# Kernel optimization log

Hardware: AMD Instinct MI355X
Metric: run time of the kernel (lower is better)

## Reference

```python
import jax, jax.numpy as jnp
import numpy as np

NUM_NODES = 50000
NUM_EDGES = 600000
NUM_FEAT = 128
HIDDEN = 512
N_OUT = 128
K = 3
N_GRAPHS = 128


def setup_inputs() -> dict:
    key = jax.random.key(0)
    ks = jax.random.split(key, 12)
    feature = jax.random.normal(ks[0], (NUM_NODES, NUM_FEAT), dtype=jnp.float32)
    edge_index = jax.random.randint(ks[1], (2, NUM_EDGES), 0, NUM_NODES, dtype=jnp.int64)
    protein_batch = jnp.sort(jax.random.randint(ks[2], (NUM_NODES,), 0, N_GRAPHS, dtype=jnp.int64))
    s = 0.05
    # ChebConv weights stored [K, in, out] (x @ W), single shared bias per conv
    W1 = jax.random.normal(ks[3], (K, NUM_FEAT, NUM_FEAT), dtype=jnp.float32) * s
    b1 = jax.random.normal(ks[4], (NUM_FEAT,), dtype=jnp.float32) * s
    W2 = jax.random.normal(ks[5], (K, NUM_FEAT, 2 * NUM_FEAT), dtype=jnp.float32) * s
    b2 = jax.random.normal(ks[6], (2 * NUM_FEAT,), dtype=jnp.float32) * s
    fc1_w = jax.random.normal(ks[7], (3 * NUM_FEAT, HIDDEN), dtype=jnp.float32) * s
    fc1_b = jax.random.normal(ks[8], (HIDDEN,), dtype=jnp.float32) * s
    fc2_w = jax.random.normal(ks[9], (HIDDEN, N_OUT), dtype=jnp.float32) * s
    fc2_b = jax.random.normal(ks[10], (N_OUT,), dtype=jnp.float32) * s
    return {"feature": feature, "edge_index": edge_index, "protein_batch": protein_batch,
            "W1": W1, "b1": b1, "W2": W2, "b2": b2,
            "fc1_w": fc1_w, "fc1_b": fc1_b, "fc2_w": fc2_w, "fc2_b": fc2_b}


def _cheb_conv(x, src, dst, edge_w, W, b):
    # PyG ChebConv with sym normalization, lambda_max=2 => scaled Laplacian
    # L_hat has zero diagonal and off-diag weights -1/sqrt(d_i d_j) (edge_w).
    def prop(h):
        return jax.ops.segment_sum(edge_w[:, None] * h[src], dst, num_segments=NUM_NODES)

    Tx0 = x
    out = Tx0 @ W[0]
    Tx1 = prop(x)
    out = out + Tx1 @ W[1]
    for k in range(2, W.shape[0]):
        Tx2 = 2.0 * prop(Tx1) - Tx0
        out = out + Tx2 @ W[k]
        Tx0, Tx1 = Tx1, Tx2
    return out + b


def reference(feature, edge_index, protein_batch, W1, b1, W2, b2, fc1_w, fc1_b, fc2_w, fc2_b):
    src, dst = edge_index[0], edge_index[1]
    deg = jax.ops.segment_sum(jnp.ones_like(src, dtype=feature.dtype), src, num_segments=NUM_NODES)
    dinv = jnp.where(deg > 0, jax.lax.rsqrt(jnp.maximum(deg, 1.0)), 0.0)
    edge_w = -dinv[src] * dinv[dst]  # (2/lambda_max)*L_sym off-diagonal; diag cancels to 0

    gx = jax.nn.relu(_cheb_conv(feature, src, dst, edge_w, W1, b1))
    gx = jax.nn.relu(_cheb_conv(gx, src, dst, edge_w, W2, b2))
    gx = jnp.concatenate([gx, feature], axis=1)  # [N, 3*F]

    # global_mean_pool
    sums = jax.ops.segment_sum(gx, protein_batch, num_segments=N_GRAPHS)
    cnts = jax.ops.segment_sum(jnp.ones((gx.shape[0],), gx.dtype), protein_batch, num_segments=N_GRAPHS)
    pooled = sums / jnp.maximum(cnts, 1.0)[:, None]

    h = jax.nn.relu(pooled @ fc1_w + fc1_b)  # dropout is identity in eval
    return h @ fc2_w + fc2_b
```

## Files before the change

kernel.cpp:

```cpp
#include <hip/hip_runtime.h>
#include <hip/hip_bf16.h>

#define NNODES 50000
#define NEDGES 600000
#define NB 196
#define NBKT 196
#define SB 192
#define SCH (NEDGES / SB)

typedef short vs8 __attribute__((ext_vector_type(8)));
typedef float floatx4 __attribute__((ext_vector_type(4)));

__device__ __forceinline__ float us2f(unsigned short u) {
    unsigned int x = ((unsigned int)u) << 16;
    float f;
    __builtin_memcpy(&f, &x, 4);
    return f;
}
__device__ __forceinline__ unsigned short f2us(float f) {
    unsigned int x;
    __builtin_memcpy(&x, &f, 4);
    unsigned int r = x + 0x7fffu + ((x >> 16) & 1u);
    return (unsigned short)(r >> 16);
}
__device__ __forceinline__ float ldf(const void* p, int i, int ff) {
    if (ff) return us2f(((const unsigned short*)p)[i]);
    return ((const float*)p)[i];
}
__device__ __forceinline__ int2 ldnt_sw(const int2* p) {
    unsigned long long v =
        __builtin_nontemporal_load(reinterpret_cast<const unsigned long long*>(p));
    int2 r;
    r.x = (int)(unsigned int)(v & 0xffffffffULL);
    r.y = (int)(unsigned int)(v >> 32);
    return r;
}
__device__ __forceinline__ void accum8(float w, uint4 u, float& a0, float& a1,
                                       float& a2, float& a3, float& a4, float& a5,
                                       float& a6, float& a7) {
    a0 += w * us2f((unsigned short)(u.x & 0xffffu));
    a1 += w * us2f((unsigned short)(u.x >> 16));
    a2 += w * us2f((unsigned short)(u.y & 0xffffu));
    a3 += w * us2f((unsigned short)(u.y >> 16));
    a4 += w * us2f((unsigned short)(u.z & 0xffffu));
    a5 += w * us2f((unsigned short)(u.z >> 16));
    a6 += w * us2f((unsigned short)(u.w & 0xffffu));
    a7 += w * us2f((unsigned short)(u.w >> 16));
}

__global__ void k_detect(const int* ei, const unsigned int* fw, int* iflag, int* fflag) {
    int lane = threadIdx.x;
    int odd1 = ei[2 * lane + 1];
    int odd2 = ei[128 + 2 * lane + 1];
    unsigned long long nz = __ballot(odd1 != 0 || odd2 != 0);
    unsigned int e = (fw[lane] >> 7) & 0xffu;
    unsigned long long h = __ballot(e > 100u && e < 160u);
    if (lane == 0) {
        *iflag = (nz == 0ULL) ? 1 : 0;
        *fflag = (__popcll(h) > 40) ? 1 : 0;
    }
}

__global__ void k_init(const int* pb, const int* iflag, int* b32, float* psum) {
    int i = blockIdx.x * 256 + threadIdx.x;
    if (i < NNODES) {
        int f = *iflag;
        b32[i] = pb[((size_t)i) << f];
    }
    if (i < 128 * 384) psum[i] = 0.f;
}

__global__ __launch_bounds__(256) void k_deghist(const int* ei, const int* iflag,
                                                 unsigned int* degpart, int* cntpart) {
    __shared__ unsigned int h[25000];
    __shared__ int c[NBKT];
    int t = threadIdx.x, blk = blockIdx.x;
    for (int i = t; i < 25000; i += 256) h[i] = 0u;
    if (t < NBKT) c[t] = 0;
    __syncthreads();
    int f = *iflag;
    int e0 = blk * SCH;
    for (int j = t; j < SCH; j += 256) {
        int e = e0 + j;
        int s = ei[((size_t)e) << f];
        int d = ei[((size_t)(NEDGES + e)) << f];
        atomicAdd(&h[s >> 1], (s & 1) ? 65536u : 1u);
        atomicAdd(&c[d >> 8], 1);
    }
    __syncthreads();
    unsigned int* dp = degpart + (size_t)blk * 25000;
    for (int i = t; i < 25000; i += 256) dp[i] = h[i];
    if (t < NBKT) cntpart[blk * NBKT + t] = c[t];
}

__global__ void k_dred(const unsigned int* degpart, float* dinv) {
    int i = blockIdx.x * 256 + threadIdx.x;
    if (i >= 25000) return;
    unsigned int lo = 0, hi = 0;
    for (int b = 0; b < SB; ++b) {
        unsigned int p = degpart[(size_t)b * 25000 + i];
        lo += p & 0xffffu;
        hi += p >> 16;
    }
    dinv[2 * i] = lo ? rsqrtf((float)lo) : 0.f;
    dinv[2 * i + 1] = hi ? rsqrtf((float)hi) : 0.f;
}

__global__ void k_bscan(const int* cntpart, int* bbase, int* gbase,
                        const int* batch32, int* pcnt, int* rowptr) {
    __shared__ int tot[256];
    int t = threadIdx.x;
    int sum = 0;
    if (t < NBKT) {
        for (int b = 0; b < SB; ++b) sum += cntpart[b * NBKT + t];
    }
    tot[t] = sum;
    __syncthreads();
    for (int off = 1; off < 256; off <<= 1) {
        int x = (t >= off) ? tot[t - off] : 0;
        __syncthreads();
        tot[t] += x;
        __syncthreads();
    }
    int excl = tot[t] - sum;
    if (t < NBKT) {
        gbase[t] = excl;
        int run = excl;
        for (int b = 0; b < SB; ++b) {
            bbase[b * NBKT + t] = run;
            run += cntpart[b * NBKT + t];
        }
    }
    if (t == 0) {
        gbase[NBKT] = NEDGES;
        rowptr[NNODES] = NEDGES;
    }
    if (t < 128) {
        int g = t;
        int lo = 0, hi = NNODES;
        while (lo < hi) { int mid = (lo + hi) >> 1; if (batch32[mid] < g) lo = mid + 1; else hi = mid; }
        int start = lo;
        hi = NNODES;
        while (lo < hi) { int mid = (lo + hi) >> 1; if (batch32[mid] <= g) lo = mid + 1; else hi = mid; }
        pcnt[g] = lo - start;
    }
}

__global__ void k_scat(const int* ei, const int* iflag, const float* dinv,
                       const int* bbase, int2* bkt) {
    __shared__ int cur[NBKT];
    int t = threadIdx.x, blk = blockIdx.x;
    if (t < NBKT) cur[t] = bbase[blk * NBKT + t];
    __syncthreads();
    int f = *iflag;
    int e0 = blk * SCH;
    for (int j = t; j < SCH; j += 256) {
        int e = e0 + j;
        int s = ei[((size_t)e) << f];
        int d = ei[((size_t)(NEDGES + e)) << f];
        float w = -dinv[s] * dinv[d];
        int slot = atomicAdd(&cur[d >> 8], 1);
        int wb;
        __builtin_memcpy(&wb, &w, 4);
        int2 v;
        v.x = s | ((d & 255) << 16);
        v.y = wb;
        bkt[slot] = v;
    }
}

__global__ void k_csr(const int2* bkt, const int* gbase, int* rowptr, int2* csr_sw) {
    __shared__ int hist[256], scan[256], cur[256];
    int t = threadIdx.x, b = blockIdx.x;
    int beg = gbase[b], end = gbase[b + 1];
    int n = end - beg;
    hist[t] = 0;
    __syncthreads();
    for (int i = t; i < n; i += 256) {
        int bin = (bkt[beg + i].x >> 16) & 255;
        atomicAdd(&hist[bin], 1);
    }
    __syncthreads();
    int h = hist[t];
    scan[t] = h;
    __syncthreads();
    for (int off = 1; off < 256; off <<= 1) {
        int x = (t >= off) ? scan[t - off] : 0;
        __syncthreads();
        scan[t] += x;
        __syncthreads();
    }
    int excl = scan[t] - h;
    int node = b * 256 + t;
    if (node < NNODES) rowptr[node] = beg + excl;
    cur[t] = excl;
    __syncthreads();
    for (int i = t; i < n; i += 256) {
        int2 p = bkt[beg + i];
        int bin = (p.x >> 16) & 255;
        int slot = atomicAdd(&cur[bin], 1);
        int2 v;
        v.x = p.x & 0xffff;
        v.y = p.y;
        csr_sw[beg + slot] = v;
    }
}

__global__ void k_featb(const void* src, const int* fflag, unsigned short* dst) {
    int i = blockIdx.x * 256 + threadIdx.x;
    if (i >= NNODES * 128 / 8) return;
    if (*fflag) {
        reinterpret_cast<uint4*>(dst)[i] = reinterpret_cast<const uint4*>(src)[i];
    } else {
        const float4* fs = reinterpret_cast<const float4*>(src);
        float4 a = fs[2 * i], b = fs[2 * i + 1];
        uint4 o;
        o.x = (unsigned int)f2us(a.x) | ((unsigned int)f2us(a.y) << 16);
        o.y = (unsigned int)f2us(a.z) | ((unsigned int)f2us(a.w) << 16);
        o.z = (unsigned int)f2us(b.x) | ((unsigned int)f2us(b.y) << 16);
        o.w = (unsigned int)f2us(b.z) | ((unsigned int)f2us(b.w) << 16);
        reinterpret_cast<uint4*>(dst)[i] = o;
    }
}

__global__ void k_trans2(const void* W1, const void* W2, const int* fflag,
                         unsigned short* W1t, unsigned short* W2t) {
    int idx = blockIdx.x * 256 + threadIdx.x;
    int ff = *fflag;
    if (idx < 49152) {
        int n = idx / 384, k = idx - n * 384;
        float v;
        if (k < 128) v = ldf(W1, k * 128 + n, ff) - ldf(W1, (256 + k) * 128 + n, ff);
        else if (k < 256) v = ldf(W1, k * 128 + n, ff);
        else v = 2.f * ldf(W1, k * 128 + n, ff);
        W1t[idx] = f2us(v);
    } else if (idx < 49152 + 98304) {
        int j = idx - 49152;
        int n = j / 384, k = j - n * 384;
        float v;
        if (k < 128) v = ldf(W2, k * 256 + n, ff) - ldf(W2, (256 + k) * 256 + n, ff);
        else if (k < 256) v = ldf(W2, k * 256 + n, ff);
        else v = 2.f * ldf(W2, k * 256 + n, ff);
        W2t[j] = f2us(v);
    }
}

__global__ void k_prepw(const void* b1, const void* b2, const void* f1w, const void* f1b,
                        const void* f2w, const void* f2b, const int* fflag,
                        float* b1f, float* b2f, float* f1wf, float* f1bf,
                        float* f2wf, float* f2bf) {
    int i = blockIdx.x * 256 + threadIdx.x;
    int ff = *fflag;
    if (i < 196608) { f1wf[i] = ldf(f1w, i, ff); return; }
    i -= 196608;
    if (i < 65536) { f2wf[i] = ldf(f2w, i, ff); return; }
    i -= 65536;
    if (i < 512) { f1bf[i] = ldf(f1b, i, ff); return; }
    i -= 512;
    if (i < 256) { b2f[i] = ldf(b2, i, ff); return; }
    i -= 256;
    if (i < 128) { b1f[i] = ldf(b1, i, ff); return; }
    i -= 128;
    if (i < 128) f2bf[i] = ldf(f2b, i, ff);
}

__global__ __launch_bounds__(256, 8) void k_prop(const unsigned short* X,
                                                 const int* rowptr, const int2* csr_sw,
                                                 unsigned short* out) {
    int wvid = (blockIdx.x * blockDim.x + threadIdx.x) >> 6;
    int lane = threadIdx.x & 63;
    int q = lane >> 4;
    int ln = lane & 15;
    int node = wvid * 4 + q;
    if (node >= NNODES) return;
    int fo = ln * 8;
    int beg = rowptr[node], end = rowptr[node + 1];
    float a0 = 0.f, a1 = 0.f, a2 = 0.f, a3 = 0.f;
    float a4 = 0.f, a5 = 0.f, a6 = 0.f, a7 = 0.f;
    int j = beg;
    for (; j + 4 <= end; j += 4) {
        int2 e0 = ldnt_sw(csr_sw + j);
        int2 e1 = ldnt_sw(csr_sw + j + 1);
        int2 e2 = ldnt_sw(csr_sw + j + 2);
        int2 e3 = ldnt_sw(csr_sw + j + 3);
        uint4 u0 = *reinterpret_cast<const uint4*>(X + (size_t)e0.x * 128 + fo);
        uint4 u1 = *reinterpret_cast<const uint4*>(X + (size_t)e1.x * 128 + fo);
        uint4 u2 = *reinterpret_cast<const uint4*>(X + (size_t)e2.x * 128 + fo);
        uint4 u3 = *reinterpret_cast<const uint4*>(X + (size_t)e3.x * 128 + fo);
        float w0, w1, w2, w3;
        __builtin_memcpy(&w0, &e0.y, 4);
        __builtin_memcpy(&w1, &e1.y, 4);
        __builtin_memcpy(&w2, &e2.y, 4);
        __builtin_memcpy(&w3, &e3.y, 4);
        accum8(w0, u0, a0, a1, a2, a3, a4, a5, a6, a7);
        accum8(w1, u1, a0, a1, a2, a3, a4, a5, a6, a7);
        accum8(w2, u2, a0, a1, a2, a3, a4, a5, a6, a7);
        accum8(w3, u3, a0, a1, a2, a3, a4, a5, a6, a7);
    }
    for (; j < end; ++j) {
        int2 e = ldnt_sw(csr_sw + j);
        float w;
        __builtin_memcpy(&w, &e.y, 4);
        uint4 u = *reinterpret_cast<const uint4*>(X + (size_t)e.x * 128 + fo);
        accum8(w, u, a0, a1, a2, a3, a4, a5, a6, a7);
    }
    uint4 ov;
    ov.x = (unsigned int)f2us(a0) | ((unsigned int)f2us(a1) << 16);
    ov.y = (unsigned int)f2us(a2) | ((unsigned int)f2us(a3) << 16);
    ov.z = (unsigned int)f2us(a4) | ((unsigned int)f2us(a5) << 16);
    ov.w = (unsigned int)f2us(a6) | ((unsigned int)f2us(a7) << 16);
    *reinterpret_cast<uint4*>(out + (size_t)node * 128 + fo) = ov;
}

template <int POOL, int NOUT>
__global__ __launch_bounds__(256, 6) void k_convg(
    const unsigned short* seg0, const unsigned short* seg1, const unsigned short* seg2,
    const unsigned short* Wt, const float* bias, unsigned short* out,
    const int* batch32, float* psum) {
    constexpr int SLABS = NOUT / 32;
    __shared__ unsigned short shb[12288];
    __shared__ float sh_ps[POOL ? 256 : 1];
    int tid = threadIdx.x;
    int bid = blockIdx.x;
    int grp = 8 * SLABS;
    int main_blocks = 24 * grp;
    int r, slab;
    if (bid < main_blocks) {
        int g = bid / grp;
        int rem = bid - g * grp;
        slab = rem >> 3;
        r = g * 8 + (rem & 7);
    } else {
        int t = bid - main_blocks;
        r = 192 + (t & 3);
        slab = t >> 2;
    }
    int col0 = slab * 32;
    if (POOL) sh_ps[tid] = 0.f;
#pragma unroll
    for (int it = 0; it < 6; ++it) {
        int idx = tid + it * 256;
        int kkt = idx >> 6, ln = idx & 63;
        int kk = kkt >> 1, t = kkt & 1;
        int col = col0 + t * 16 + (ln & 15);
        int ko = kk * 32 + (ln >> 4) * 8;
        uint4 v = *reinterpret_cast<const uint4*>(Wt + (size_t)col * 384 + ko);
        *reinterpret_cast<uint4*>(shb + idx * 8) = v;
    }
    __syncthreads();
    int wv = tid >> 6, lane = tid & 63;
    int m = lane & 15, kq = lane >> 4;
    int row0 = r * 256 + wv * 64;
    int rr[4];
#pragma unroll
    for (int mt = 0; mt < 4; ++mt) {
        int rw = row0 + mt * 16 + m;
        rr[mt] = rw < NNODES ? rw : NNODES - 1;
    }
    floatx4 acc[4][2];
#pragma unroll
    for (int mt = 0; mt < 4; ++mt)
#pragma unroll
        for (int t = 0; t < 2; ++t) {
            acc[mt][t][0] = 0.f; acc[mt][t][1] = 0.f;
            acc[mt][t][2] = 0.f; acc[mt][t][3] = 0.f;
        }
    const unsigned short* segs[3];
    segs[0] = seg0; segs[1] = seg1; segs[2] = seg2;
#pragma unroll
    for (int kk = 0; kk < 12; ++kk) {
        const unsigned short* S = segs[kk >> 2];
        int ko = (kk & 3) * 32 + kq * 8;
        vs8 a[4];
#pragma unroll
        for (int mt = 0; mt < 4; ++mt)
            a[mt] = *reinterpret_cast<const vs8*>(S + (size_t)rr[mt] * 128 + ko);
#pragma unroll
        for (int t = 0; t < 2; ++t) {
            vs8 b = *reinterpret_cast<const vs8*>(shb + ((kk * 2 + t) * 64 + lane) * 8);
#pragma unroll
            for (int mt = 0; mt < 4; ++mt)
                acc[mt][t] = __builtin_amdgcn_mfma_f32_16x16x32_bf16(a[mt], b, acc[mt][t], 0, 0, 0);
        }
    }
    if (POOL == 0) {
#pragma unroll
        for (int mt = 0; mt < 4; ++mt) {
            int rbase = row0 + mt * 16 + kq * 4;
#pragma unroll
            for (int t = 0; t < 2; ++t) {
                int col = col0 + t * 16 + m;
                float bv = bias[col];
#pragma unroll
                for (int i = 0; i < 4; ++i) {
                    int rw = rbase + i;
                    if (rw < NNODES) {
                        float v = acc[mt][t][i] + bv;
                        v = v > 0.f ? v : 0.f;
                        out[(size_t)rw * NOUT + col] = f2us(v);
                    }
                }
            }
        }
    } else {
        int g0 = batch32[r * 256];
#pragma unroll
        for (int mt = 0; mt < 4; ++mt) {
            int rbase = row0 + mt * 16 + kq * 4;
            int gid[4];
#pragma unroll
            for (int i = 0; i < 4; ++i) {
                int rw = rbase + i;
                gid[i] = rw < NNODES ? batch32[rw] : -1;
            }
#pragma unroll
            for (int t = 0; t < 2; ++t) {
                int col = col0 + t * 16 + m;
                float bv = bias[col];
                float run = 0.f;
                int curg = -1;
#pragma unroll
                for (int i = 0; i < 4; ++i) {
                    int g = gid[i];
                    if (g < 0) break;
                    float v = acc[mt][t][i] + bv;
                    v = v > 0.f ? v : 0.f;
                    if (g != curg) {
                        if (curg >= 0) {
                            int gl = curg - g0;
                            if (gl >= 0 && gl < 8) atomicAdd(&sh_ps[gl * 32 + t * 16 + m], run);
                            else atomicAdd(&psum[curg * 384 + col], run);
                        }
                        curg = g;
                        run = 0.f;
                    }
                    run += v;
                }
                if (curg >= 0) {
                    int gl = curg - g0;
                    if (gl >= 0 && gl < 8) atomicAdd(&sh_ps[gl * 32 + t * 16 + m], run);
                    else atomicAdd(&psum[curg * 384 + col], run);
                }
            }
        }
        __syncthreads();
        int gl = tid >> 5, c = tid & 31;
        float v = sh_ps[tid];
        int gg = g0 + gl;
        if (v != 0.f && gg < 128) atomicAdd(&psum[(size_t)gg * 384 + col0 + c], v);
    }
}

__global__ void k_poolnodes(const unsigned short* featb, const int* batch32, float* psum) {
    int col = threadIdx.x & 127;
    int half = threadIdx.x >> 7;
    int nbeg = blockIdx.x * 128 + half * 64;
    if (nbeg >= NNODES) return;
    int nend = nbeg + 64;
    if (nend > NNODES) nend = NNODES;
    float run = 0.f;
    int curg = batch32[nbeg];
    for (int n = nbeg; n < nend; ++n) {
        int g = batch32[n];
        if (g != curg) {
            atomicAdd(&psum[curg * 384 + 256 + col], run);
            run = 0.f;
            curg = g;
        }
        run += us2f(featb[(size_t)n * 128 + col]);
    }
    atomicAdd(&psum[curg * 384 + 256 + col], run);
}

__global__ void k_fc1(const float* psum, const int* pcnt, const float* w,
                      const float* b, float* h) {
    int g = blockIdx.x, j = threadIdx.x * 2;
    int c = pcnt[g];
    float inv = 1.f / (float)(c > 0 ? c : 1);
    float a0 = 0.f, a1 = 0.f;
    for (int k = 0; k < 384; ++k) {
        float p = psum[g * 384 + k];
        a0 += p * w[k * 512 + j];
        a1 += p * w[k * 512 + j + 1];
    }
    a0 = a0 * inv + b[j];
    a1 = a1 * inv + b[j + 1];
    h[g * 512 + j] = a0 > 0.f ? a0 : 0.f;
    h[g * 512 + j + 1] = a1 > 0.f ? a1 : 0.f;
}

__global__ void ChebModel_74380243632480_kernel(const float* h, const float* w,
                                                const float* b, const int* fflag,
                                                void* out) {
    int g = blockIdx.x, j = threadIdx.x;
    float acc = 0.f;
    for (int k = 0; k < 512; ++k) acc += h[g * 512 + k] * w[k * 128 + j];
    acc += b[j];
    if (*fflag) ((unsigned short*)out)[g * 128 + j] = f2us(acc);
    else ((float*)out)[g * 128 + j] = acc;
}

extern "C" void kernel_launch(void* const* d_in, const int* in_sizes, int n_in,
                              void* d_out, int out_size, void* d_ws, size_t ws_size,
                              hipStream_t stream) {
    const void* feature = d_in[0];
    const int* edge_index = (const int*)d_in[1];
    const int* batch = (const int*)d_in[2];
    const void* W1 = d_in[3];
    const void* b1 = d_in[4];
    const void* W2 = d_in[5];
    const void* b2 = d_in[6];
    const void* fc1w = d_in[7];
    const void* fc1b = d_in[8];
    const void* fc2w = d_in[9];
    const void* fc2b = d_in[10];

    char* ws = (char*)d_ws;
    size_t off = 0;
    int* iflag = (int*)(ws + off); off += 256;
    int* fflag = (int*)(ws + off); off += 256;
    int* rowptr = (int*)(ws + off); off += ((size_t)(NNODES + 1) * 4 + 255) & ~(size_t)255;
    float* dinv = (float*)(ws + off); off += ((size_t)NNODES * 4 + 255) & ~(size_t)255;
    int* batch32 = (int*)(ws + off); off += ((size_t)NNODES * 4 + 255) & ~(size_t)255;
    int* gbase = (int*)(ws + off); off += 1024;
    int* cntpart = (int*)(ws + off); off += ((size_t)SB * NBKT * 4 + 255) & ~(size_t)255;
    int* bbase = (int*)(ws + off); off += ((size_t)SB * NBKT * 4 + 255) & ~(size_t)255;
    int2* csr_sw = (int2*)(ws + off); off += ((size_t)NEDGES * 8 + 255) & ~(size_t)255;
    unsigned short* featb = (unsigned short*)(ws + off); off += ((size_t)NNODES * 128 * 2 + 255) & ~(size_t)255;
    unsigned short* T1 = (unsigned short*)(ws + off); off += ((size_t)NNODES * 128 * 2 + 255) & ~(size_t)255;
    unsigned short* T2 = (unsigned short*)(ws + off); off += ((size_t)NNODES * 128 * 2 + 255) & ~(size_t)255;
    unsigned short* gx1 = (unsigned short*)(ws + off); off += ((size_t)NNODES * 128 * 2 + 255) & ~(size_t)255;
    unsigned short* W1t = (unsigned short*)(ws + off); off += ((size_t)49152 * 2 + 255) & ~(size_t)255;
    unsigned short* W2t = (unsigned short*)(ws + off); off += ((size_t)98304 * 2 + 255) & ~(size_t)255;
    float* b1f = (float*)(ws + off); off += 1024;
    float* b2f = (float*)(ws + off); off += 1024;
    float* fc1wf = (float*)(ws + off); off += ((size_t)196608 * 4 + 255) & ~(size_t)255;
    float* fc1bf = (float*)(ws + off); off += 2048;
    float* fc2wf = (float*)(ws + off); off += ((size_t)65536 * 4 + 255) & ~(size_t)255;
    float* fc2bf = (float*)(ws + off); off += 1024;
    float* psum = (float*)(ws + off); off += ((size_t)128 * 384 * 4 + 255) & ~(size_t)255;
    int* pcnt = (int*)(ws + off); off += 1024;
    float* hbuf = (float*)(ws + off); off += ((size_t)128 * 512 * 4 + 255) & ~(size_t)255;

    int2* bkt = (int2*)T1;
    unsigned int* degpart = (unsigned int*)T2;

    k_detect<<<1, 64, 0, stream>>>(edge_index, (const unsigned int*)feature, iflag, fflag);
    k_init<<<(NNODES + 255) / 256, 256, 0, stream>>>(batch, iflag, batch32, psum);
    k_deghist<<<SB, 256, 0, stream>>>(edge_index, iflag, degpart, cntpart);
    k_dred<<<(25000 + 255) / 256, 256, 0, stream>>>(degpart, dinv);
    k_bscan<<<1, 256, 0, stream>>>(cntpart, bbase, gbase, batch32, pcnt, rowptr);
    k_scat<<<SB, 256, 0, stream>>>(edge_index, iflag, dinv, bbase, bkt);
    k_csr<<<NBKT, 256, 0, stream>>>(bkt, gbase, rowptr, csr_sw);

    k_featb<<<(NNODES * 128 / 8 + 255) / 256, 256, 0, stream>>>(feature, fflag, featb);
    k_trans2<<<(49152 + 98304 + 255) / 256, 256, 0, stream>>>(W1, W2, fflag, W1t, W2t);
    k_prepw<<<(263168 + 255) / 256, 256, 0, stream>>>(b1, b2, fc1w, fc1b, fc2w, fc2b, fflag,
                                                      b1f, b2f, fc1wf, fc1bf, fc2wf, fc2bf);

    int pb = ((NNODES + 3) / 4 * 64 + 255) / 256;
    k_prop<<<pb, 256, 0, stream>>>(featb, rowptr, csr_sw, T1);
    k_prop<<<pb, 256, 0, stream>>>(T1, rowptr, csr_sw, T2);
    k_convg<0, 128><<<24 * 32 + 16, 256, 0, stream>>>(featb, T1, T2, W1t, b1f, gx1,
                                                      (const int*)0, (float*)0);
    k_prop<<<pb, 256, 0, stream>>>(gx1, rowptr, csr_sw, T1);
    k_prop<<<pb, 256, 0, stream>>>(T1, rowptr, csr_sw, T2);
    k_convg<1, 256><<<24 * 64 + 32, 256, 0, stream>>>(gx1, T1, T2, W2t, b2f, (unsigned short*)0,
                                                      batch32, psum);
    k_poolnodes<<<(NNODES + 127) / 128, 256, 0, stream>>>(featb, batch32, psum);
    k_fc1<<<128, 256, 0, stream>>>(psum, pcnt, fc1wf, fc1bf, hbuf);
    ChebModel_74380243632480_kernel<<<128, 128, 0, stream>>>(hbuf, fc2wf, fc2bf, fflag, d_out);
}
```

Baseline: 421.6 us.

## Retile Chebyshev GEMM to 128x128 tiles with double-buffered async LDS staging

```diff
diff --git a/kernel.cpp b/kernel.cpp
--- a/kernel.cpp
+++ b/kernel.cpp
@@ -34,6 +34,11 @@
     r.x = (int)(unsigned int)(v & 0xffffffffULL);
     r.y = (int)(unsigned int)(v >> 32);
     return r;
+}
+__device__ __forceinline__ void gload_lds16(const unsigned short* g, unsigned short* l) {
+    __builtin_amdgcn_global_load_lds(
+        (const __attribute__((address_space(1))) unsigned int*)g,
+        (__attribute__((address_space(3))) unsigned int*)l, 16, 0, 0);
 }
 __device__ __forceinline__ void accum8(float w, uint4 u, float& a0, float& a1,
                                        float& a2, float& a3, float& a4, float& a5,
@@ -228,20 +233,34 @@
     int idx = blockIdx.x * 256 + threadIdx.x;
     int ff = *fflag;
     if (idx < 49152) {
-        int n = idx / 384, k = idx - n * 384;
+        int c = idx >> 13;
+        int rem = idx & 8191;
+        int cr = rem >> 6;
+        int rem2 = rem & 63;
+        int g = rem2 >> 3, j = rem2 & 7;
+        int k = c * 64 + ((g ^ (cr & 7)) << 3) + j;
+        int n = cr;
         float v;
         if (k < 128) v = ldf(W1, k * 128 + n, ff) - ldf(W1, (256 + k) * 128 + n, ff);
         else if (k < 256) v = ldf(W1, k * 128 + n, ff);
         else v = 2.f * ldf(W1, k * 128 + n, ff);
         W1t[idx] = f2us(v);
     } else if (idx < 49152 + 98304) {
-        int j = idx - 49152;
-        int n = j / 384, k = j - n * 384;
+        int jx = idx - 49152;
+        int ct = jx / 49152;
+        int rem = jx % 49152;
+        int c = rem >> 13;
+        int rem1 = rem & 8191;
+        int cr = rem1 >> 6;
+        int rem2 = rem1 & 63;
+        int g = rem2 >> 3, j = rem2 & 7;
+        int k = c * 64 + ((g ^ (cr & 7)) << 3) + j;
+        int n = ct * 128 + cr;
         float v;
         if (k < 128) v = ldf(W2, k * 256 + n, ff) - ldf(W2, (256 + k) * 256 + n, ff);
         else if (k < 256) v = ldf(W2, k * 256 + n, ff);
         else v = 2.f * ldf(W2, k * 256 + n, ff);
-        W2t[j] = f2us(v);
+        W2t[jx] = f2us(v);
     }
 }
 
@@ -312,101 +331,125 @@
     *reinterpret_cast<uint4*>(out + (size_t)node * 128 + fo) = ov;
 }
 
-template <int POOL, int NOUT>
-__global__ __launch_bounds__(256, 6) void k_convg(
+template <int POOL, int CT>
+__global__ __launch_bounds__(512, 4) void k_convg(
     const unsigned short* seg0, const unsigned short* seg1, const unsigned short* seg2,
     const unsigned short* Wt, const float* bias, unsigned short* out,
     const int* batch32, float* psum) {
-    constexpr int SLABS = NOUT / 32;
-    __shared__ unsigned short shb[12288];
-    __shared__ float sh_ps[POOL ? 256 : 1];
+    __shared__ __align__(16) unsigned short a_lds[2][8192];
+    __shared__ __align__(16) unsigned short b_lds[2][8192];
+    __shared__ float sh_ps[POOL ? 1024 : 1];
     int tid = threadIdx.x;
     int bid = blockIdx.x;
-    int grp = 8 * SLABS;
-    int main_blocks = 24 * grp;
-    int r, slab;
+    int grp = 8 * CT;
+    int main_blocks = 48 * grp;
+    int r, ct;
     if (bid < main_blocks) {
         int g = bid / grp;
         int rem = bid - g * grp;
-        slab = rem >> 3;
+        ct = rem >> 3;
         r = g * 8 + (rem & 7);
     } else {
         int t = bid - main_blocks;
-        r = 192 + (t & 3);
-        slab = t >> 2;
-    }
-    int col0 = slab * 32;
-    if (POOL) sh_ps[tid] = 0.f;
-#pragma unroll
-    for (int it = 0; it < 6; ++it) {
-        int idx = tid + it * 256;
-        int kkt = idx >> 6, ln = idx & 63;
-        int kk = kkt >> 1, t = kkt & 1;
-        int col = col0 + t * 16 + (ln & 15);
-        int ko = kk * 32 + (ln >> 4) * 8;
-        uint4 v = *reinterpret_cast<const uint4*>(Wt + (size_t)col * 384 + ko);
-        *reinterpret_cast<uint4*>(shb + idx * 8) = v;
-    }
-    __syncthreads();
+        r = 384 + (CT == 1 ? t : t % 7);
+        ct = (CT == 1) ? 0 : t / 7;
+    }
+    int r0 = r * 128;
+    const unsigned short* segs[3] = {seg0, seg1, seg2};
     int wv = tid >> 6, lane = tid & 63;
+    int wm = wv >> 2, wn = wv & 3;
     int m = lane & 15, kq = lane >> 4;
-    int row0 = r * 256 + wv * 64;
-    int rr[4];
-#pragma unroll
-    for (int mt = 0; mt < 4; ++mt) {
-        int rw = row0 + mt * 16 + m;
-        rr[mt] = rw < NNODES ? rw : NNODES - 1;
-    }
+    if (POOL) { sh_ps[tid] = 0.f; sh_ps[tid + 512] = 0.f; }
+
+    auto STAGE = [&](int buf, int c) {
+        const unsigned short* S = segs[c >> 1];
+        int h = c & 1;
+#pragma unroll
+        for (int p = 0; p < 2; ++p) {
+            int q = wv * 2 + p;
+            int rl = q * 8 + (lane >> 3);
+            int g = lane & 7;
+            int rowg = r0 + rl;
+            if (rowg >= NNODES) rowg = NNODES - 1;
+            gload_lds16(S + (size_t)rowg * 128 + h * 64 + ((g ^ (rl & 7)) << 3),
+                        &a_lds[buf][q * 512]);
+        }
+#pragma unroll
+        for (int p = 0; p < 2; ++p) {
+            int q = wv * 2 + p;
+            gload_lds16(Wt + (size_t)(ct * 6 + c) * 8192 + q * 512 + (lane << 3),
+                        &b_lds[buf][q * 512]);
+        }
+    };
+
     floatx4 acc[4][2];
 #pragma unroll
     for (int mt = 0; mt < 4; ++mt)
 #pragma unroll
-        for (int t = 0; t < 2; ++t) {
-            acc[mt][t][0] = 0.f; acc[mt][t][1] = 0.f;
-            acc[mt][t][2] = 0.f; acc[mt][t][3] = 0.f;
-        }
-    const unsigned short* segs[3];
-    segs[0] = seg0; segs[1] = seg1; segs[2] = seg2;
-#pragma unroll
-    for (int kk = 0; kk < 12; ++kk) {
-        const unsigned short* S = segs[kk >> 2];
-        int ko = (kk & 3) * 32 + kq * 8;
-        vs8 a[4];
-#pragma unroll
-        for (int mt = 0; mt < 4; ++mt)
-            a[mt] = *reinterpret_cast<const vs8*>(S + (size_t)rr[mt] * 128 + ko);
-#pragma unroll
-        for (int t = 0; t < 2; ++t) {
-            vs8 b = *reinterpret_cast<const vs8*>(shb + ((kk * 2 + t) * 64 + lane) * 8);
+        for (int nt = 0; nt < 2; ++nt) {
+            acc[mt][nt][0] = 0.f; acc[mt][nt][1] = 0.f;
+            acc[mt][nt][2] = 0.f; acc[mt][nt][3] = 0.f;
+        }
+
+    STAGE(0, 0);
+    __syncthreads();
+    int buf = 0;
+#pragma unroll
+    for (int c = 0; c < 6; ++c) {
+        if (c < 5) STAGE(buf ^ 1, c + 1);
+        vs8 af[4], bfr[2];
+#pragma unroll
+        for (int kf = 0; kf < 2; ++kf) {
+            int G = kf * 4 + kq;
+#pragma unroll
+            for (int mt = 0; mt < 4; ++mt) {
+                int row = wm * 64 + mt * 16 + m;
+                af[mt] = *reinterpret_cast<const vs8*>(
+                    &a_lds[buf][row * 64 + ((G ^ (row & 7)) << 3)]);
+            }
+#pragma unroll
+            for (int nt = 0; nt < 2; ++nt) {
+                int cl = wn * 32 + nt * 16 + m;
+                bfr[nt] = *reinterpret_cast<const vs8*>(
+                    &b_lds[buf][cl * 64 + ((G ^ (cl & 7)) << 3)]);
+            }
 #pragma unroll
             for (int mt = 0; mt < 4; ++mt)
-                acc[mt][t] = __builtin_amdgcn_mfma_f32_16x16x32_bf16(a[mt], b, acc[mt][t], 0, 0, 0);
-        }
-    }
+#pragma unroll
+                for (int nt = 0; nt < 2; ++nt)
+                    acc[mt][nt] = __builtin_amdgcn_mfma_f32_16x16x32_bf16(
+                        af[mt], bfr[nt], acc[mt][nt], 0, 0, 0);
+        }
+        if (c < 5) {
+            __syncthreads();
+            buf ^= 1;
+        }
+    }
+
     if (POOL == 0) {
 #pragma unroll
         for (int mt = 0; mt < 4; ++mt) {
-            int rbase = row0 + mt * 16 + kq * 4;
-#pragma unroll
-            for (int t = 0; t < 2; ++t) {
-                int col = col0 + t * 16 + m;
+            int rbase = r0 + wm * 64 + mt * 16 + kq * 4;
+#pragma unroll
+            for (int nt = 0; nt < 2; ++nt) {
+                int col = wn * 32 + nt * 16 + m;
                 float bv = bias[col];
 #pragma unroll
                 for (int i = 0; i < 4; ++i) {
                     int rw = rbase + i;
                     if (rw < NNODES) {
-                        float v = acc[mt][t][i] + bv;
+                        float v = acc[mt][nt][i] + bv;
                         v = v > 0.f ? v : 0.f;
-                        out[(size_t)rw * NOUT + col] = f2us(v);
+                        out[(size_t)rw * 128 + col] = f2us(v);
                     }
                 }
             }
         }
     } else {
-        int g0 = batch32[r * 256];
+        int g0 = batch32[r0];
 #pragma unroll
         for (int mt = 0; mt < 4; ++mt) {
-            int rbase = row0 + mt * 16 + kq * 4;
+            int rbase = r0 + wm * 64 + mt * 16 + kq * 4;
             int gid[4];
 #pragma unroll
             for (int i = 0; i < 4; ++i) {
@@ -414,8 +457,9 @@
                 gid[i] = rw < NNODES ? batch32[rw] : -1;
             }
 #pragma unroll
-            for (int t = 0; t < 2; ++t) {
-                int col = col0 + t * 16 + m;
+            for (int nt = 0; nt < 2; ++nt) {
+                int cl = wn * 32 + nt * 16 + m;
+                int col = ct * 128 + cl;
                 float bv = bias[col];
                 float run = 0.f;
                 int curg = -1;
@@ -423,12 +467,12 @@
                 for (int i = 0; i < 4; ++i) {
                     int g = gid[i];
                     if (g < 0) break;
-                    float v = acc[mt][t][i] + bv;
+                    float v = acc[mt][nt][i] + bv;
                     v = v > 0.f ? v : 0.f;
                     if (g != curg) {
                         if (curg >= 0) {
                             int gl = curg - g0;
-                            if (gl >= 0 && gl < 8) atomicAdd(&sh_ps[gl * 32 + t * 16 + m], run);
+                            if (gl >= 0 && gl < 8) atomicAdd(&sh_ps[gl * 128 + cl], run);
                             else atomicAdd(&psum[curg * 384 + col], run);
                         }
                         curg = g;
@@ -438,16 +482,18 @@
                 }
                 if (curg >= 0) {
                     int gl = curg - g0;
-                    if (gl >= 0 && gl < 8) atomicAdd(&sh_ps[gl * 32 + t * 16 + m], run);
+                    if (gl >= 0 && gl < 8) atomicAdd(&sh_ps[gl * 128 + cl], run);
                     else atomicAdd(&psum[curg * 384 + col], run);
                 }
             }
         }
         __syncthreads();
-        int gl = tid >> 5, c = tid & 31;
-        float v = sh_ps[tid];
-        int gg = g0 + gl;
-        if (v != 0.f && gg < 128) atomicAdd(&psum[(size_t)gg * 384 + col0 + c], v);
+        for (int idx = tid; idx < 1024; idx += 512) {
+            int gl = idx >> 7, cl = idx & 127;
+            float v = sh_ps[idx];
+            int gg = g0 + gl;
+            if (v != 0.f && gg < 128) atomicAdd(&psum[(size_t)gg * 384 + ct * 128 + cl], v);
+        }
     }
 }
 
@@ -561,12 +607,12 @@
     int pb = ((NNODES + 3) / 4 * 64 + 255) / 256;
     k_prop<<<pb, 256, 0, stream>>>(featb, rowptr, csr_sw, T1);
     k_prop<<<pb, 256, 0, stream>>>(T1, rowptr, csr_sw, T2);
-    k_convg<0, 128><<<24 * 32 + 16, 256, 0, stream>>>(featb, T1, T2, W1t, b1f, gx1,
-                                                      (const int*)0, (float*)0);
+    k_convg<0, 1><<<391, 512, 0, stream>>>(featb, T1, T2, W1t, b1f, gx1,
+                                           (const int*)0, (float*)0);
     k_prop<<<pb, 256, 0, stream>>>(gx1, rowptr, csr_sw, T1);
     k_prop<<<pb, 256, 0, stream>>>(T1, rowptr, csr_sw, T2);
-    k_convg<1, 256><<<24 * 64 + 32, 256, 0, stream>>>(gx1, T1, T2, W2t, b2f, (unsigned short*)0,
-                                                      batch32, psum);
+    k_convg<1, 2><<<782, 512, 0, stream>>>(gx1, T1, T2, W2t, b2f, (unsigned short*)0,
+                                           batch32, psum);
     k_poolnodes<<<(NNODES + 127) / 128, 256, 0, stream>>>(featb, batch32, psum);
     k_fc1<<<128, 256, 0, stream>>>(psum, pcnt, fc1wf, fc1bf, hbuf);
     ChebModel_74380243632480_kernel<<<128, 128, 0, stream>>>(hbuf, fc2wf, fc2bf, fflag, d_out);
```

Result: faster. 393.1 us (-6.8%).
